# Kernel tuning notes

Hardware: AMD Instinct MI355X
Metric: run time of the kernel (lower is better)

The kernel has to match this reference:

```python
import jax, jax.numpy as jnp
import numpy as np

USER_NUM = 100000
ITEM_NUM = 50000
N_NODES = USER_NUM + ITEM_NUM
EMB = 64
N_LAYERS = 3
N_EDGES = 4000000


def setup_inputs() -> dict:
    key = jax.random.key(0)
    k1, k2, k3, k4, k5 = jax.random.split(key, 5)
    user_emb = jax.random.normal(k1, (USER_NUM, EMB), dtype=jnp.float32)
    item_emb = jax.random.normal(k2, (ITEM_NUM, EMB), dtype=jnp.float32)
    # COO sparse normalized adjacency (values would be 1/sqrt(deg_u*deg_v) in the real graph)
    edge_vals = jax.random.uniform(k3, (N_EDGES,), dtype=jnp.float32)
    edge_src = jax.random.randint(k4, (N_EDGES,), 0, N_NODES, dtype=jnp.int32)
    edge_dst = jax.random.randint(k5, (N_EDGES,), 0, N_NODES, dtype=jnp.int32)
    return {"user_emb": user_emb, "item_emb": item_emb, "edge_vals": edge_vals,
            "edge_src": edge_src, "edge_dst": edge_dst}


def reference(user_emb, item_emb, edge_vals, edge_src, edge_dst):
    # emb = cat([user_emb, item_emb])  -> [N, d]
    emb = jnp.concatenate([user_emb, item_emb], axis=0)
    acc = emb  # running sum over layer embeddings (fuses stack+mean)
    for _ in range(N_LAYERS):
        # SpMM: (A @ emb) via gather -> scale -> segment scatter-add
        msg = edge_vals[:, None] * emb[edge_src]          # [E, d]
        emb = jax.ops.segment_sum(msg, edge_dst, num_segments=N_NODES)
        acc = acc + emb
    final_emb = acc / jnp.float32(N_LAYERS + 1)            # mean over L+1 layer embeddings
    # original returns (final_emb[:user_num], final_emb[user_num:], all_emb);
    # user/item split is a trivial slice of this single array
    return final_emb
```

## Files before the change

kernel.cpp:

```cpp
#include <hip/hip_runtime.h>
#include <hip/hip_fp16.h>

constexpr int USER_NUM = 100000;
constexpr int ITEM_NUM = 50000;
constexpr int N_NODES  = USER_NUM + ITEM_NUM;
constexpr int EMB      = 64;
constexpr int N_LAYERS = 3;
constexpr int NB       = (N_NODES + 255) >> 8;
constexpr int TILE     = 2048;
constexpr int CAP      = 8184;


__device__ inline unsigned pack_f16_2(float a, float b) {
    __half2 h = __floats2half2_rn(a, b);
    return __builtin_bit_cast(unsigned, h);
}

__device__ inline float2 unp_f16_2(unsigned u) {
    return __half22float2(__builtin_bit_cast(__half2, u));
}

__device__ inline void hfma4(uint4 u, __half2 v, __half2* a) {
    a[0] = __hfma2(__builtin_bit_cast(__half2, u.x), v, a[0]);
    a[1] = __hfma2(__builtin_bit_cast(__half2, u.y), v, a[1]);
    a[2] = __hfma2(__builtin_bit_cast(__half2, u.z), v, a[2]);
    a[3] = __hfma2(__builtin_bit_cast(__half2, u.w), v, a[3]);
}


__global__ __launch_bounds__(256) void init_f16_k(const float4* __restrict__ user,
                                                  const float4* __restrict__ item,
                                                  uint4* __restrict__ embA,
                                                  int total8, int user8) {
    int g = blockIdx.x * 256 + threadIdx.x;
    if (g >= total8) return;
    const float4* s4;
    int base;
    if (g < user8) { s4 = user; base = g * 2; }
    else           { s4 = item; base = (g - user8) * 2; }
    float4 lo = s4[base];
    float4 hi = s4[base + 1];
    uint4 o;
    o.x = pack_f16_2(lo.x, lo.y);
    o.y = pack_f16_2(lo.z, lo.w);
    o.z = pack_f16_2(hi.x, hi.y);
    o.w = pack_f16_2(hi.z, hi.w);
    embA[g] = o;
}


__global__ __launch_bounds__(256) void partition_k(const float* __restrict__ vals,
                                                   const int* __restrict__ src,
                                                   const int* __restrict__ dst,
                                                   int* __restrict__ gcursor,
                                                   unsigned* __restrict__ rkey,
                                                   unsigned short* __restrict__ rvalq,
                                                   int n_edges) {
    __shared__ int lcnt[NB];
    __shared__ int gb[NB];
    int tid = threadIdx.x;
    int base = blockIdx.x * TILE;
    int n = min(TILE, n_edges - base);

    for (int b = tid; b < NB; b += 256) lcnt[b] = 0;
    __syncthreads();

    unsigned key[8];
    int rel[8];
    short bk[8];
    #pragma unroll
    for (int j = 0; j < 8; ++j) {
        int k = j * 256 + tid;
        if (k < n) {
            int e = base + k;
            int d = dst[e];
            int b = d >> 8;
            key[j] = (unsigned)src[e] | ((unsigned)(d & 255) << 18);
            bk[j]  = (short)b;
            rel[j] = atomicAdd(&lcnt[b], 1);
        } else bk[j] = -1;
    }
    __syncthreads();

    for (int b = tid; b < NB; b += 256) {
        int c = lcnt[b];
        if (c > 0) gb[b] = atomicAdd(&gcursor[b], c);
    }
    __syncthreads();

    #pragma unroll
    for (int j = 0; j < 8; ++j) {
        if (bk[j] >= 0) {
            int pos = gb[bk[j]] + rel[j];
            if (pos < CAP) {
                size_t idx = (size_t)bk[j] * CAP + pos;
                int e = base + j * 256 + tid;
                rkey[idx]  = key[j];
                rvalq[idx] = (unsigned short)min((unsigned)(vals[e] * 16384.0f + 0.5f), 16383u);
            }
        }
    }
}

__global__ __launch_bounds__(512) void csrfin_k(const int* __restrict__ gcursor,
                                                const unsigned* __restrict__ rkey,
                                                const unsigned short* __restrict__ rvalq,
                                                unsigned* __restrict__ pairs,
                                                int* __restrict__ rowbeg,
                                                int* __restrict__ rowend) {
    __shared__ int lhist[256];
    __shared__ int lcur[256];
    __shared__ int wsum[4];
    int b = blockIdx.x;
    int node_base = b << 8;
    int nn = min(256, N_NODES - node_base);
    int tid = threadIdx.x;
    int cnt = min(gcursor[b], CAP);
    int rbase = b * CAP;

    if (tid < 256) lhist[tid] = 0;
    __syncthreads();
    for (int i = tid; i < cnt; i += 512)
        atomicAdd(&lhist[rkey[rbase + i] >> 18], 1);
    __syncthreads();

    if (tid < 256) {
        int lane = tid & 63, wid = tid >> 6;
        int v = lhist[tid];
        int x = v;
        #pragma unroll
        for (int off = 1; off < 64; off <<= 1) {
            int y = __shfl_up(x, off);
            if (lane >= off) x += y;
        }
        if (lane == 63) wsum[wid] = x;
        __syncthreads();
        if (tid == 0) {
            int c = 0;
            #pragma unroll
            for (int j = 0; j < 4; ++j) { int t = wsum[j]; wsum[j] = c; c += t; }
        }
        __syncthreads();
        int excl = wsum[wid] + x - v;
        if (tid < nn) {
            rowbeg[node_base + tid] = rbase + excl;
            rowend[node_base + tid] = rbase + excl + v;
            lcur[tid] = rbase + excl;
        }
    } else {
        __syncthreads();
        __syncthreads();
    }
    __syncthreads();

    for (int i = tid; i < cnt; i += 512) {
        unsigned k = rkey[rbase + i];
        unsigned valq = rvalq[rbase + i];
        int local = (int)(k >> 18);
        unsigned s = k & 0x3FFFFu;
        int pos = atomicAdd(&lcur[local], 1);
        pairs[pos] = s | (valq << 18);
    }
}


template <int LAST>
__global__ __launch_bounds__(256) void gather_k(const int* __restrict__ rowbeg,
                                                const int* __restrict__ rowend,
                                                const unsigned* __restrict__ pairs,
                                                const uint4* __restrict__ emb,
                                                uint4* __restrict__ nxt,
                                                float4* __restrict__ outf,
                                                const uint4* __restrict__ e1,
                                                const uint4* __restrict__ e2,
                                                const float4* __restrict__ user,
                                                const float4* __restrict__ item) {
    int wid  = threadIdx.x >> 6;
    int node = blockIdx.x * 4 + wid;
    if (node >= N_NODES) return;
    int lane = threadIdx.x & 63;
    int sub  = lane >> 3;
    int q    = lane & 7;

    int beg = rowbeg[node];
    int end = rowend[node];

    __half2 h0[4], h1[4], h2[4], h3[4];
    #pragma unroll
    for (int j = 0; j < 4; ++j) {
        h0[j] = __float2half2_rn(0.0f);
        h1[j] = __float2half2_rn(0.0f);
        h2[j] = __float2half2_rn(0.0f);
        h3[j] = __float2half2_rn(0.0f);
    }

    const float kInv = 1.0f / 16384.0f;
    for (int p = beg; p < end; p += 32) {
        int i0 = p + sub, i1 = p + 8 + sub, i2 = p + 16 + sub, i3 = p + 24 + sub;
        unsigned u0 = (i0 < end) ? pairs[i0] : 0u;
        unsigned u1 = (i1 < end) ? pairs[i1] : 0u;
        unsigned u2 = (i2 < end) ? pairs[i2] : 0u;
        unsigned u3 = (i3 < end) ? pairs[i3] : 0u;
        uint4 x0 = emb[(size_t)(u0 & 0x3FFFFu) * 8 + q];
        uint4 x1 = emb[(size_t)(u1 & 0x3FFFFu) * 8 + q];
        uint4 x2 = emb[(size_t)(u2 & 0x3FFFFu) * 8 + q];
        uint4 x3 = emb[(size_t)(u3 & 0x3FFFFu) * 8 + q];
        hfma4(x0, __float2half2_rn((float)(u0 >> 18) * kInv), h0);
        hfma4(x1, __float2half2_rn((float)(u1 >> 18) * kInv), h1);
        hfma4(x2, __float2half2_rn((float)(u2 >> 18) * kInv), h2);
        hfma4(x3, __float2half2_rn((float)(u3 >> 18) * kInv), h3);
    }

    float s[8];
    #pragma unroll
    for (int j = 0; j < 4; ++j) {
        float2 f0 = __half22float2(h0[j]);
        float2 f1 = __half22float2(h1[j]);
        float2 f2 = __half22float2(h2[j]);
        float2 f3 = __half22float2(h3[j]);
        s[2 * j]     = (f0.x + f1.x) + (f2.x + f3.x);
        s[2 * j + 1] = (f0.y + f1.y) + (f2.y + f3.y);
    }
    #pragma unroll
    for (int j = 0; j < 8; ++j) {
        float t = s[j];
        t += __shfl_xor(t, 8);
        t += __shfl_xor(t, 16);
        t += __shfl_xor(t, 32);
        s[j] = t;
    }

    if (sub == 0) {
        if (LAST) {
            int fb = node * 16 + q * 2;
            float4 u0 = (node < USER_NUM) ? user[fb]     : item[(node - USER_NUM) * 16 + q * 2];
            float4 u1 = (node < USER_NUM) ? user[fb + 1] : item[(node - USER_NUM) * 16 + q * 2 + 1];
            uint4 b1 = e1[(size_t)node * 8 + q];
            uint4 b2 = e2[(size_t)node * 8 + q];
            float2 a1[4], a2[4];
            a1[0] = unp_f16_2(b1.x); a1[1] = unp_f16_2(b1.y);
            a1[2] = unp_f16_2(b1.z); a1[3] = unp_f16_2(b1.w);
            a2[0] = unp_f16_2(b2.x); a2[1] = unp_f16_2(b2.y);
            a2[2] = unp_f16_2(b2.z); a2[3] = unp_f16_2(b2.w);
            float4 r0, r1;
            r0.x = (u0.x + a1[0].x + a2[0].x + s[0]) * 0.25f;
            r0.y = (u0.y + a1[0].y + a2[0].y + s[1]) * 0.25f;
            r0.z = (u0.z + a1[1].x + a2[1].x + s[2]) * 0.25f;
            r0.w = (u0.w + a1[1].y + a2[1].y + s[3]) * 0.25f;
            r1.x = (u1.x + a1[2].x + a2[2].x + s[4]) * 0.25f;
            r1.y = (u1.y + a1[2].y + a2[2].y + s[5]) * 0.25f;
            r1.z = (u1.z + a1[3].x + a2[3].x + s[6]) * 0.25f;
            r1.w = (u1.w + a1[3].y + a2[3].y + s[7]) * 0.25f;
            outf[fb]     = r0;
            outf[fb + 1] = r1;
        } else {
            uint4 o;
            o.x = pack_f16_2(s[0], s[1]);
            o.y = pack_f16_2(s[2], s[3]);
            o.z = pack_f16_2(s[4], s[5]);
            o.w = pack_f16_2(s[6], s[7]);
            nxt[(size_t)node * 8 + q] = o;
        }
    }
}


__global__ __launch_bounds__(256) void fb_init_k(const float4* __restrict__ user,
                                                 const float4* __restrict__ item,
                                                 float4* __restrict__ embA,
                                                 float4* __restrict__ acc,
                                                 int total4, int user4) {
    int i = blockIdx.x * 256 + threadIdx.x;
    if (i >= total4) return;
    float4 v = (i < user4) ? user[i] : item[i - user4];
    embA[i] = v;
    acc[i]  = v;
}

__global__ __launch_bounds__(256) void scatter_k(const float* __restrict__ emb,
                                                 const float* __restrict__ vals,
                                                 const int*   __restrict__ src,
                                                 const int*   __restrict__ dst,
                                                 float* __restrict__ out,
                                                 int n_edges) {
    long long gtid = (long long)blockIdx.x * 256 + threadIdx.x;
    int e = (int)(gtid >> 4);
    if (e >= n_edges) return;
    int lane = (int)(gtid & 15);
    float v = vals[e];
    float4 x = ((const float4*)(emb + (size_t)src[e] * EMB))[lane];
    float* o = out + (size_t)dst[e] * EMB + (size_t)lane * 4;
    unsafeAtomicAdd(o + 0, v * x.x);
    unsafeAtomicAdd(o + 1, v * x.y);
    unsafeAtomicAdd(o + 2, v * x.z);
    unsafeAtomicAdd(o + 3, v * x.w);
}

__global__ __launch_bounds__(256) void acc_k(float4* __restrict__ acc,
                                             const float4* __restrict__ emb, int total4) {
    int i = blockIdx.x * 256 + threadIdx.x;
    if (i >= total4) return;
    float4 a = acc[i], b = emb[i];
    a.x += b.x; a.y += b.y; a.z += b.z; a.w += b.w;
    acc[i] = a;
}

__global__ __launch_bounds__(256) void scale_k(float4* __restrict__ acc, float s, int total4) {
    int i = blockIdx.x * 256 + threadIdx.x;
    if (i >= total4) return;
    float4 a = acc[i];
    a.x *= s; a.y *= s; a.z *= s; a.w *= s;
    acc[i] = a;
}

extern "C" void kernel_launch(void* const* d_in, const int* in_sizes, int n_in,
                              void* d_out, int out_size, void* d_ws, size_t ws_size,
                              hipStream_t stream) {
    const float* user = (const float*)d_in[0];
    const float* item = (const float*)d_in[1];
    const float* vals = (const float*)d_in[2];
    const int*   src  = (const int*)d_in[3];
    const int*   dst  = (const int*)d_in[4];
    float* out = (float*)d_out;

    const int n_edges = in_sizes[2];
    const size_t embf32_bytes = (size_t)N_NODES * EMB * sizeof(float);
    const size_t embf16_bytes = (size_t)N_NODES * EMB * 2;

    const int total4 = N_NODES * EMB / 4;
    const int user4  = USER_NUM * EMB / 4;
    const int total8 = N_NODES * EMB / 8;
    const int user8  = USER_NUM * EMB / 8;
    const int blocks_e4 = (total4 + 255) / 256;
    const int blocks_e8 = (total8 + 255) / 256;

    size_t off = 0;
    uint4*    bufA  = (uint4*)((char*)d_ws + off); off += embf16_bytes;
    uint4*    bufB  = (uint4*)((char*)d_ws + off); off += embf16_bytes;
    uint4*    bufC  = (uint4*)((char*)d_ws + off); off += embf16_bytes;
    unsigned* pairs = (unsigned*)((char*)d_ws + off); off += (size_t)NB * CAP * sizeof(unsigned);
    int*      rowbeg= (int*)((char*)d_ws + off); off += (size_t)N_NODES * sizeof(int);
    int*      rowend= (int*)((char*)d_ws + off); off += (size_t)N_NODES * sizeof(int);
    int*      gcursor=(int*)((char*)d_ws + off); off += (size_t)NB * sizeof(int);

    unsigned*       rkey  = (unsigned*)bufB;
    unsigned short* rvalq = (unsigned short*)bufC;

    if (ws_size < off || n_edges >= (1 << 22)) {
        float* fA = (float*)d_ws;
        float* fB = (float*)((char*)d_ws + embf32_bytes);
        fb_init_k<<<blocks_e4, 256, 0, stream>>>((const float4*)user, (const float4*)item,
                                                 (float4*)fA, (float4*)out, total4, user4);
        const long long work = (long long)n_edges * 16;
        const int blocks_s = (int)((work + 255) / 256);
        float* cur = fA; float* nxt = fB;
        for (int l = 0; l < N_LAYERS; ++l) {
            hipMemsetAsync(nxt, 0, embf32_bytes, stream);
            scatter_k<<<blocks_s, 256, 0, stream>>>(cur, vals, src, dst, nxt, n_edges);
            acc_k<<<blocks_e4, 256, 0, stream>>>((float4*)out, (const float4*)nxt, total4);
            float* t = cur; cur = nxt; nxt = t;
        }
        scale_k<<<blocks_e4, 256, 0, stream>>>((float4*)out, 1.0f / (N_LAYERS + 1), total4);
        return;
    }

    const int blocks_p = (n_edges + TILE - 1) / TILE;
    hipMemsetAsync(gcursor, 0, (size_t)NB * sizeof(int), stream);
    partition_k<<<blocks_p, 256, 0, stream>>>(vals, src, dst, gcursor, rkey, rvalq, n_edges);
    csrfin_k<<<NB, 512, 0, stream>>>(gcursor, rkey, rvalq, pairs, rowbeg, rowend);

    init_f16_k<<<blocks_e8, 256, 0, stream>>>((const float4*)user, (const float4*)item,
                                              bufA, total8, user8);

    const int blocks_g = (N_NODES + 3) / 4;
    gather_k<0><<<blocks_g, 256, 0, stream>>>(rowbeg, rowend, pairs, bufA, bufB, nullptr,
                                              nullptr, nullptr, nullptr, nullptr);
    gather_k<0><<<blocks_g, 256, 0, stream>>>(rowbeg, rowend, pairs, bufB, bufC, nullptr,
                                              nullptr, nullptr, nullptr, nullptr);
    gather_k<1><<<blocks_g, 256, 0, stream>>>(rowbeg, rowend, pairs, bufC, nullptr, (float4*)out,
                                              bufB, bufC,
                                              (const float4*)user, (const float4*)item);
}
```

Before: 400.7 us.

## Stage partitioned edges in LDS sorted by bucket before global scatter

Measured after the change: 345.6 us. 13.7% less time.

```diff
diff --git a/kernel.cpp b/kernel.cpp
--- a/kernel.cpp
+++ b/kernel.cpp
@@ -56,17 +56,21 @@
                                                    unsigned* __restrict__ rkey,
                                                    unsigned short* __restrict__ rvalq,
                                                    int n_edges) {
-    __shared__ int lcnt[NB];
+    __shared__ int lhist[NB];
+    __shared__ int loff[NB];
+    __shared__ int lcur[NB];
     __shared__ int gb[NB];
+    __shared__ unsigned long long stage[TILE];
+
     int tid = threadIdx.x;
     int base = blockIdx.x * TILE;
     int n = min(TILE, n_edges - base);
 
-    for (int b = tid; b < NB; b += 256) lcnt[b] = 0;
+    for (int b = tid; b < NB; b += 256) lhist[b] = 0;
     __syncthreads();
 
     unsigned key[8];
-    int rel[8];
+    unsigned short vq[8];
     short bk[8];
     #pragma unroll
     for (int j = 0; j < 8; ++j) {
@@ -76,28 +80,56 @@
             int d = dst[e];
             int b = d >> 8;
             key[j] = (unsigned)src[e] | ((unsigned)(d & 255) << 18);
+            vq[j]  = (unsigned short)min((unsigned)(vals[e] * 16384.0f + 0.5f), 16383u);
             bk[j]  = (short)b;
-            rel[j] = atomicAdd(&lcnt[b], 1);
+            atomicAdd(&lhist[b], 1);
         } else bk[j] = -1;
     }
     __syncthreads();
 
-    for (int b = tid; b < NB; b += 256) {
-        int c = lcnt[b];
-        if (c > 0) gb[b] = atomicAdd(&gcursor[b], c);
+    if (tid < 64) {
+        int carry = 0;
+        #pragma unroll
+        for (int c = 0; c < (NB + 63) / 64; ++c) {
+            int idx = c * 64 + tid;
+            int v = (idx < NB) ? lhist[idx] : 0;
+            int x = v;
+            #pragma unroll
+            for (int off = 1; off < 64; off <<= 1) {
+                int y = __shfl_up(x, off);
+                if (tid >= off) x += y;
+            }
+            if (idx < NB) { loff[idx] = carry + x - v; lcur[idx] = carry + x - v; }
+            carry += __shfl(x, 63);
+        }
     }
     __syncthreads();
 
     #pragma unroll
     for (int j = 0; j < 8; ++j) {
         if (bk[j] >= 0) {
-            int pos = gb[bk[j]] + rel[j];
-            if (pos < CAP) {
-                size_t idx = (size_t)bk[j] * CAP + pos;
-                int e = base + j * 256 + tid;
-                rkey[idx]  = key[j];
-                rvalq[idx] = (unsigned short)min((unsigned)(vals[e] * 16384.0f + 0.5f), 16383u);
-            }
+            int slot = atomicAdd(&lcur[bk[j]], 1);
+            stage[slot] = (unsigned long long)key[j]
+                        | ((unsigned long long)vq[j] << 26)
+                        | ((unsigned long long)(unsigned)bk[j] << 40);
+        }
+    }
+    __syncthreads();
+
+    for (int b = tid; b < NB; b += 256) {
+        int c = lcur[b] - loff[b];
+        if (c > 0) gb[b] = atomicAdd(&gcursor[b], c);
+    }
+    __syncthreads();
+
+    for (int slot = tid; slot < n; slot += 256) {
+        unsigned long long rec = stage[slot];
+        int b = (int)(rec >> 40);
+        int pos = gb[b] + (slot - loff[b]);
+        if (pos < CAP) {
+            size_t idx = (size_t)b * CAP + pos;
+            rkey[idx]  = (unsigned)(rec & 0x3FFFFFFu);
+            rvalq[idx] = (unsigned short)((rec >> 26) & 0x3FFFu);
         }
     }
 }
```
